# Performance work log

Hardware: AMD Instinct MI355X
Metric: run time of the kernel (lower is better)

Reference implementation:

```python
import jax, jax.numpy as jnp
import numpy as np
import math

K, T, B, N = 16, 40, 16, 32
BN = B * N


def _conv(x, w, b, stride):
    y = jax.lax.conv_general_dilated(x, w, (stride, stride), [(2, 2), (2, 2)],
                                     dimension_numbers=('NCHW', 'OIHW', 'NCHW'))
    return y + b[None, :, None, None]


def setup_inputs() -> dict:
    key = jax.random.key(0)
    ks = jax.random.split(key, 20)
    inp = {
        'hx': jax.random.normal(ks[0], (BN, 48), jnp.float32),
        'current_location': jax.random.uniform(ks[1], (BN, 2), jnp.float32, 0.0, 40.0),
        'y_path': jax.random.uniform(ks[2], (K, T, BN, 2), jnp.float32, 0.0, 40.0),
        'image_data': jax.random.normal(ks[3], (B, 4, 160, 160), jnp.float32),
        'conv1_w': jax.random.normal(ks[4], (16, 4, 5, 5), jnp.float32) * 0.1,
        'conv1_b': jax.random.normal(ks[5], (16,), jnp.float32) * 0.1,
        'conv2_w': jax.random.normal(ks[6], (32, 16, 5, 5), jnp.float32) * 0.05,
        'conv2_b': jax.random.normal(ks[7], (32,), jnp.float32) * 0.1,
        'fc_vel_w': jax.random.normal(ks[8], (16, 2), jnp.float32) * 0.1,
        'fc_vel_b': jax.random.normal(ks[9], (16,), jnp.float32) * 0.1,
        'fc_scf_w': jax.random.normal(ks[10], (48, 1728), jnp.float32) * 0.02,
        'fc_scf_b': jax.random.normal(ks[11], (48,), jnp.float32) * 0.1,
        'gru_w_ih': jax.random.normal(ks[12], (144, 96), jnp.float32) * 0.1,
        'gru_w_hh': jax.random.normal(ks[13], (144, 48), jnp.float32) * 0.1,
        'gru_b_ih': jax.random.normal(ks[14], (144,), jnp.float32) * 0.1,
        'gru_b_hh': jax.random.normal(ks[15], (144,), jnp.float32) * 0.1,
        'fc_dy_w': jax.random.normal(ks[16], (80, 48), jnp.float32) * 0.1,
        'fc_dy_b': jax.random.normal(ks[17], (80,), jnp.float32) * 0.1,
        'fc_score_w': jax.random.normal(ks[18], (1, 48), jnp.float32) * 0.1,
        'fc_score_b': jax.random.normal(ks[19], (1,), jnp.float32) * 0.1,
    }
    return inp


def reference(hx, current_location, y_path, image_data, conv1_w, conv1_b, conv2_w, conv2_b,
              fc_vel_w, fc_vel_b, fc_scf_w, fc_scf_b, gru_w_ih, gru_w_hh, gru_b_ih, gru_b_hh,
              fc_dy_w, fc_dy_b, fc_score_w, fc_score_b):
    k, t, bn, _ = y_path.shape
    b = image_data.shape[0]
    n = bn // b
    HZ = 10.0
    R0, R1 = 0.5, 4.0
    r_step = (R1 - R0) / 6.0
    th_step = 2.0 * math.pi / 6.0

    fmap = jax.nn.relu(_conv(jax.nn.relu(_conv(image_data, conv1_w, conv1_b, 2)), conv2_w, conv2_b, 1))  # (B,32,80,80)
    H, W = fmap.shape[2], fmap.shape[3]
    fm = fmap.transpose(0, 2, 3, 1)  # (B,H,W,32)

    # velocities (detached in original)
    vel = jnp.concatenate([y_path[:, :1] - current_location[None, None], jnp.diff(y_path, axis=1)], axis=1) * HZ
    vel = jax.lax.stop_gradient(vel)
    y_fv = vel @ fc_vel_w.T + fc_vel_b  # (K,T,bn,16)

    h0 = jnp.tile(hx, (k, 1))  # (K*bn,48)
    b_idx = jnp.arange(b)[None, :, None]
    eye = jnp.eye(n, dtype=bool)[None, None]

    def step(h, inp):
        path_t, fv_t = inp  # (K,bn,2), (K,bn,16)
        P = path_t.reshape(k, b, n, 2)  # bn index = batch*n + agent
        # map-feature gather at agent pixel
        u = jnp.clip(H // 2 - P[..., 1].astype(jnp.int32), 0, H - 1)
        v = jnp.clip(P[..., 0].astype(jnp.int32), 0, W - 1)
        feat = fm[b_idx, u, v]  # (K,B,N,32)
        # radius/theta binning (indices detached in original)
        Pd = jax.lax.stop_gradient(P)
        c = Pd[:, :, None, :, :] - Pd[:, :, :, None, :]  # c[k,b,j,t] = other_t - agent_j
        dist = jnp.linalg.norm(c, axis=-1)  # (K,B,N,N)
        mask = (dist >= R0) & (dist <= R1) & (~eye)
        dc = jnp.where(dist < 1e-10, 1e-10, dist)
        costh = jnp.arccos(jnp.clip(c[..., 0] / dc, -1.0, 1.0))
        theta = jnp.where(c[..., 1] < -0.01, 2.0 * math.pi - costh, costh)
        ub = jnp.clip(((dist - R0) / r_step).astype(jnp.int32), 0, 5)
        vb = jnp.clip((theta / th_step).astype(jnp.int32), 0, 5)
        bins = ub * 6 + vb  # (K,B,N,N) in [0,36)
        onehot = jax.nn.one_hot(bins, 36, dtype=h.dtype) * mask[..., None].astype(h.dtype)
        Hn = h[:bn].reshape(b, n, 48)  # original indexes only first bn rows of hidden
        sp = jnp.einsum('kbjto,bth->kbjoh', onehot, Hn)  # scatter-by-bin sum
        cnt = jnp.maximum(jnp.sum(onehot, axis=3), 1.0)
        sp = sp / jax.lax.stop_gradient(cnt)[..., None]
        sps = sp.reshape(k, bn, 36 * 48)
        lhalf = jnp.concatenate([feat, fv_t.reshape(k, b, n, 16)], axis=-1).reshape(k, bn, 48)
        rhalf = sps @ fc_scf_w.T + fc_scf_b
        x = jnp.concatenate([lhalf, rhalf], axis=-1).reshape(k * bn, 96)
        gi = x @ gru_w_ih.T + gru_b_ih
        gh = h @ gru_w_hh.T + gru_b_hh
        r = jax.nn.sigmoid(gi[:, :48] + gh[:, :48])
        z = jax.nn.sigmoid(gi[:, 48:96] + gh[:, 48:96])
        nn_ = jnp.tanh(gi[:, 96:] + r * gh[:, 96:])
        h_new = (1.0 - z) * nn_ + z * h
        return h_new, h_new

    path_seq = jnp.moveaxis(y_path, 1, 0)  # (T,K,bn,2)
    fv_seq = jnp.moveaxis(y_fv, 1, 0)
    h_final, hs = jax.lax.scan(step, h0, (path_seq, fv_seq))

    delta_y = (h_final @ fc_dy_w.T + fc_dy_b).reshape(k, bn, 2, t).transpose(0, 3, 1, 2)  # (K,T,bn,2)
    score = jnp.sum(hs @ fc_score_w.T + fc_score_b, axis=0).reshape(k, bn, 1)
    return delta_y, score
```

## Files before the change

### kernel.cpp

```cpp
#include <hip/hip_runtime.h>
#include <math.h>

typedef unsigned char u8;

#define KK 16
#define TT 40
#define BB 16
#define NN 32
#define BN 512
#define KBN 8192

#define OFF_FM   0u
#define OFF_C1   3276800u
#define OFF_W2T  4915200u
#define OFF_WT9  4928000u
#define OFF_WH3  4948736u
#define OFF_WGT  4951040u
#define OFF_H0   5033984u
#define OFF_H1   5427200u
#define OFF_SC   5820416u

__global__ __launch_bounds__(256) void k_init(const float* hx, float* h, float* score){
  int idx = blockIdx.x*256 + threadIdx.x;
  if (idx < KBN*48) h[idx] = hx[idx % (BN*48)];
  if (idx < KBN) score[idx] = 0.f;
}

__global__ __launch_bounds__(256) void k_prep(const float* conv2_w, const float* scfw,
                                              const float* wih, const float* whh,
                                              float* w2t, float* wt9g, float* wh3g, float* wgt_g){
  int idx = blockIdx.x*256 + threadIdx.x;
  if (idx < 12800) {
    int oc = idx & 31; int rest = idx >> 5;
    w2t[idx] = conv2_w[oc*400 + rest];
  }
  int i2 = idx - 12800;
  if (i2 >= 0 && i2 < 20736) {
    int kk2 = i2 / 144, rem = i2 % 144;
    int c = rem / 3, g = rem % 3;
    int o = g*48 + c;
    wt9g[i2] = (kk2 < 96) ? wih[o*96 + kk2] : whh[o*48 + (kk2 - 96)];
  }
  int i3 = idx - 33536;
  if (i3 >= 0 && i3 < 2304) {
    int kk2s = i3 / 48, c = i3 % 48;
    wh3g[i3] = whh[(96 + c)*48 + kk2s];
  }
  int i4 = idx - 35840;
  if (i4 >= 0 && i4 < 82944) {
    int bin = i4 / 2304, r2 = i4 % 2304;
    int hh = r2 / 48, cc = r2 % 48;
    wgt_g[i4] = scfw[cc*1728 + bin*48 + hh];
  }
}

__global__ __launch_bounds__(256) void k_conv1(const float* img, const float* w1, const float* b1, float* c1){
  int idx = blockIdx.x*256 + threadIdx.x;
  int ow = idx % 80, t1 = idx / 80;
  int oh = t1 % 80, t2 = t1 / 80;
  int oc = t2 % 16, b = t2 / 16;
  float acc = b1[oc];
  for (int ic = 0; ic < 4; ++ic)
    for (int kh = 0; kh < 5; ++kh) {
      int ih = oh*2 - 2 + kh;
      if (ih < 0 || ih >= 160) continue;
      const float* ip = img + ((b*4 + ic)*160 + ih)*160;
      const float* wp = w1 + ((oc*4 + ic)*5 + kh)*5;
      #pragma unroll
      for (int kw = 0; kw < 5; ++kw) {
        int iw = ow*2 - 2 + kw;
        if (iw >= 0 && iw < 160) acc += ip[iw] * wp[kw];
      }
    }
  c1[idx] = fmaxf(acc, 0.f);
}

__global__ __launch_bounds__(256) void k_conv2(const float* c1, const float* w2t, const float* b2, float* fm){
  int idx = blockIdx.x*256 + threadIdx.x;
  int oc = idx & 31;
  int t1 = idx >> 5;
  int owg = t1 % 20; int t2 = t1 / 20;
  int oh = t2 % 80; int b = t2 / 80;
  int ow0 = owg*4;
  float acc0=b2[oc],acc1=b2[oc],acc2=b2[oc],acc3=b2[oc];
  for (int ic = 0; ic < 16; ++ic)
    for (int kh = 0; kh < 5; ++kh) {
      int ih = oh - 2 + kh;
      if (ih < 0 || ih >= 80) continue;
      const float* ip = c1 + ((b*16 + ic)*80 + ih)*80;
      float cv[8];
      #pragma unroll
      for (int q = 0; q < 8; ++q) {
        int iw = ow0 - 2 + q;
        cv[q] = (iw >= 0 && iw < 80) ? ip[iw] : 0.f;
      }
      const float* wp = w2t + (ic*25 + kh*5)*32 + oc;
      #pragma unroll
      for (int kw = 0; kw < 5; ++kw) {
        float wv = wp[kw*32];
        acc0 += cv[kw]   * wv;
        acc1 += cv[kw+1] * wv;
        acc2 += cv[kw+2] * wv;
        acc3 += cv[kw+3] * wv;
      }
    }
  float* op = fm + ((b*80 + oh)*80 + ow0)*32 + oc;
  op[0]  = fmaxf(acc0, 0.f);
  op[32] = fmaxf(acc1, 0.f);
  op[64] = fmaxf(acc2, 0.f);
  op[96] = fmaxf(acc3, 0.f);
}

__global__ __launch_bounds__(256) void k_step2(
    const float* __restrict__ y_path, const float* __restrict__ cur_loc,
    const float* __restrict__ fm, const float* __restrict__ wgt,
    const float* __restrict__ wt9g,
    const float* __restrict__ vw, const float* __restrict__ vb2,
    const float* __restrict__ scfb, const float* __restrict__ bih,
    const float* __restrict__ bhh, const float* __restrict__ scw,
    const float* __restrict__ scb, const float* __restrict__ dyw,
    const float* __restrict__ dyb,
    const float* __restrict__ hin, float* __restrict__ hout,
    float* __restrict__ score, float* __restrict__ out, int t)
{
  __align__(16) __shared__ float wts[23040];
  __shared__ float X[32][148];
  __shared__ float HnL[32][49];
  __shared__ float PXs[32], PYs[32];
  __shared__ u8 BINM[32][32];
  __shared__ int PLE[1024];
  __shared__ float PWL[1024];
  __shared__ float SROW[32];
  __shared__ int lcnt;

  int tid = threadIdx.x;
  int row0 = blockIdx.x * 32;
  int kk = blockIdx.x >> 4;
  int bb = blockIdx.x & 15;

  {
    const float4* src = reinterpret_cast<const float4*>(wt9g);
    float4* dst = reinterpret_cast<float4*>(wts);
    for (int i = tid; i < 5760; i += 256) dst[i] = src[i];
  }
  for (int i = tid; i < 1536; i += 256) { int r = i/48, c = i%48; X[r][96+c] = hin[(row0+r)*48 + c]; }
  for (int i = tid; i < 1536; i += 256) { int r = i/48, c = i%48; HnL[r][c] = hin[(bb*32+r)*48 + c]; }
  if (tid < 32) {
    PXs[tid] = y_path[((kk*TT + t)*BN + bb*32 + tid)*2];
    PYs[tid] = y_path[((kk*TT + t)*BN + bb*32 + tid)*2 + 1];
    SROW[tid] = 0.f;
  }
  if (tid == 0) lcnt = 0;
  __syncthreads();

  for (int it2 = 0; it2 < 4; ++it2) {
    int p = tid + it2*256;
    int j = p >> 5, q = p & 31;
    float dx = PXs[q] - PXs[j], dy = PYs[q] - PYs[j];
    float dist = sqrtf(dx*dx + dy*dy);
    int bin = 255;
    if (q != j && dist >= 0.5f && dist <= 4.0f) {
      float ct = fminf(1.f, fmaxf(-1.f, dx / dist));
      float costh = acosf(ct);
      float theta = (dy < -0.01f) ? (6.28318530717958647692f - costh) : costh;
      int ub = (int)((dist - 0.5f) / 0.58333331346511840820f);
      ub = min(max(ub, 0), 5);
      int vb = (int)(theta / 1.04719758033752441406f);
      vb = min(max(vb, 0), 5);
      bin = ub*6 + vb;
    }
    BINM[j][q] = (u8)bin;
  }
  __syncthreads();

  for (int it2 = 0; it2 < 4; ++it2) {
    int p = tid + it2*256;
    int j = p >> 5, q = p & 31;
    int bq = BINM[j][q];
    if (bq != 255) {
      int cnt2 = 0;
      #pragma unroll
      for (int q2 = 0; q2 < 32; ++q2) cnt2 += (BINM[j][q2] == bq) ? 1 : 0;
      int idx2 = atomicAdd(&lcnt, 1);
      PLE[idx2] = (bq << 16) | (j << 8) | q;
      PWL[idx2] = 1.0f / (float)cnt2;
    }
  }
  for (int it2 = 0; it2 < 12; ++it2) {
    int task = tid + it2*256;
    int r = task / 96, c = task % 96;
    int rr = (row0 + r) & 511;
    float val;
    if (c < 32) {
      int u = min(max(40 - (int)PYs[r], 0), 79);
      int v = min(max((int)PXs[r], 0), 79);
      val = fm[((bb*80 + u)*80 + v)*32 + c];
    } else if (c < 48) {
      int o = c - 32;
      float qx, qy;
      if (t == 0) { qx = cur_loc[rr*2]; qy = cur_loc[rr*2 + 1]; }
      else { qx = y_path[((kk*TT + t - 1)*BN + rr)*2]; qy = y_path[((kk*TT + t - 1)*BN + rr)*2 + 1]; }
      float vx = (PXs[r] - qx)*10.f, vy = (PYs[r] - qy)*10.f;
      val = vx*vw[o*2] + vy*vw[o*2 + 1] + vb2[o];
    } else {
      val = scfb[c - 48];
    }
    X[r][c] = val;
  }
  __syncthreads();

  int P = lcnt;
  {
    int wid = tid >> 6, lane = tid & 63;
    if (lane < 48) {
      for (int p = wid; p < P; p += 4) {
        int e = PLE[p];
        int bin = e >> 16, j = (e >> 8) & 31, q = e & 31;
        float wv = PWL[p];
        const float* wp = wgt + bin*2304 + lane;
        float acc = 0.f;
        #pragma unroll
        for (int hh = 0; hh < 48; ++hh) acc += HnL[q][hh] * wp[hh*48];
        atomicAdd(&X[j][48 + lane], wv * acc);
      }
    }
  }
  __syncthreads();

  const float* wt9 = wts;
  const float* wh3 = wts + 20736;
  int tx = tid & 15, ty = tid >> 4;
  int r0 = ty*2;
  float a9[2][9], a3[2][3];
  #pragma unroll
  for (int ri = 0; ri < 2; ++ri) {
    #pragma unroll
    for (int m = 0; m < 9; ++m) a9[ri][m] = 0.f;
    #pragma unroll
    for (int m = 0; m < 3; ++m) a3[ri][m] = 0.f;
  }
  for (int k2 = 0; k2 < 144; ++k2) {
    float x0 = X[r0][k2], x1 = X[r0+1][k2];
    const float* wr = wt9 + k2*144 + 9*tx;
    #pragma unroll
    for (int m = 0; m < 9; ++m) {
      float wvm = wr[m];
      a9[0][m] += x0*wvm;
      a9[1][m] += x1*wvm;
    }
  }
  for (int k2 = 0; k2 < 48; ++k2) {
    float x0 = X[r0][96+k2], x1 = X[r0+1][96+k2];
    const float* wr = wh3 + k2*48 + 3*tx;
    #pragma unroll
    for (int m = 0; m < 3; ++m) {
      float wvm = wr[m];
      a3[0][m] += x0*wvm;
      a3[1][m] += x1*wvm;
    }
  }
  float hn[2][3];
  #pragma unroll
  for (int ri = 0; ri < 2; ++ri)
    #pragma unroll
    for (int c3 = 0; c3 < 3; ++c3) {
      int c = 3*tx + c3;
      float gR = a9[ri][3*c3+0] + bih[c]    + bhh[c];
      float gZ = a9[ri][3*c3+1] + bih[48+c] + bhh[48+c];
      float gN = a9[ri][3*c3+2] + bih[96+c] + bhh[96+c];
      float g3 = a3[ri][c3] + bhh[96+c];
      float rg = 1.f/(1.f + expf(-gR));
      float zg = 1.f/(1.f + expf(-gZ));
      float nn2 = tanhf(gN + (rg - 1.f)*g3);
      float hold = X[r0+ri][96+c];
      hn[ri][c3] = (1.f - zg)*nn2 + zg*hold;
    }
  __syncthreads();

  float sp0 = 0.f, sp1 = 0.f;
  #pragma unroll
  for (int c3 = 0; c3 < 3; ++c3) {
    int c = 3*tx + c3;
    X[r0][96+c]   = hn[0][c3];
    X[r0+1][96+c] = hn[1][c3];
    hout[(row0+r0)*48 + c]   = hn[0][c3];
    hout[(row0+r0+1)*48 + c] = hn[1][c3];
    sp0 += hn[0][c3]*scw[c];
    sp1 += hn[1][c3]*scw[c];
  }
  atomicAdd(&SROW[r0], sp0);
  atomicAdd(&SROW[r0+1], sp1);
  __syncthreads();

  if (tid < 32) {
    float s = score[row0 + tid] + SROW[tid] + scb[0];
    score[row0 + tid] = s;
    if (t == TT-1) out[KBN*80 + row0 + tid] = s;
  }
  if (t == TT-1) {
    for (int it2 = 0; it2 < 10; ++it2) {
      int task = tid + it2*256;
      int r = task / 80, c = task % 80;
      float acc = dyb[c];
      #pragma unroll
      for (int i = 0; i < 48; ++i) acc += X[r][96+i] * dyw[c*48 + i];
      int rr = (row0 + r) & 511;
      int d = c / 40, tq = c % 40;
      out[((kk*40 + tq)*512 + rr)*2 + d] = acc;
    }
  }
}

extern "C" void kernel_launch(void* const* d_in, const int* in_sizes, int n_in,
                              void* d_out, int out_size, void* d_ws, size_t ws_size,
                              hipStream_t stream)
{
  const float* hx   = (const float*)d_in[0];
  const float* cl   = (const float*)d_in[1];
  const float* yp   = (const float*)d_in[2];
  const float* img  = (const float*)d_in[3];
  const float* w1   = (const float*)d_in[4];
  const float* b1   = (const float*)d_in[5];
  const float* w2   = (const float*)d_in[6];
  const float* b2   = (const float*)d_in[7];
  const float* vw   = (const float*)d_in[8];
  const float* vb   = (const float*)d_in[9];
  const float* scfw = (const float*)d_in[10];
  const float* scfb = (const float*)d_in[11];
  const float* wih  = (const float*)d_in[12];
  const float* whh  = (const float*)d_in[13];
  const float* bih  = (const float*)d_in[14];
  const float* bhh  = (const float*)d_in[15];
  const float* dyw  = (const float*)d_in[16];
  const float* dyb  = (const float*)d_in[17];
  const float* scw  = (const float*)d_in[18];
  const float* scb  = (const float*)d_in[19];

  float* ws   = (float*)d_ws;
  float* fm   = ws + OFF_FM;
  float* c1   = ws + OFF_C1;
  float* w2t  = ws + OFF_W2T;
  float* wt9g = ws + OFF_WT9;
  float* wh3g = ws + OFF_WH3;
  float* wgtg = ws + OFF_WGT;
  float* hb0  = ws + OFF_H0;
  float* hb1  = ws + OFF_H1;
  float* sc   = ws + OFF_SC;
  float* out  = (float*)d_out;

  hipLaunchKernelGGL(k_init,  dim3(1536), dim3(256), 0, stream, hx, hb0, sc);
  hipLaunchKernelGGL(k_prep,  dim3(464),  dim3(256), 0, stream, w2, scfw, wih, whh, w2t, wt9g, wh3g, wgtg);
  hipLaunchKernelGGL(k_conv1, dim3(6400), dim3(256), 0, stream, img, w1, b1, c1);
  hipLaunchKernelGGL(k_conv2, dim3(3200), dim3(256), 0, stream, c1, w2t, b2, fm);
  for (int t = 0; t < TT; ++t) {
    float* hin  = (t & 1) ? hb1 : hb0;
    float* hout = (t & 1) ? hb0 : hb1;
    hipLaunchKernelGGL(k_step2, dim3(256), dim3(256), 0, stream,
        yp, cl, fm, wgtg, wt9g, vw, vb, scfb, bih, bhh, scw, scb, dyw, dyb, hin, hout, sc, out, t);
  }
}
```

Baseline: 1.761 ms.

## Fuse all GRU time steps into one persistent kernel with redundant k=0 chain

Replaces the 40 per-step launches with a single kernel that loops over time inside each block. Every step reads the hidden state of the k=0 rows, so each block now carries a second 32-row copy of that k=0 recurrence alongside its own rows. This removes the cross-block dependency, along with the global hidden-state ping-pong buffers and the init kernel. Weights and biases are loaded into shared memory once instead of every step, and the score is accumulated in registers. The cost is roughly twice the GRU and social-pooling arithmetic per block, plus higher register pressure from the 4-row tiles.

New measurement: 4.462 ms. +153.3%, slower.

```diff
diff --git a/kernel.cpp b/kernel.cpp
--- a/kernel.cpp
+++ b/kernel.cpp
@@ -16,15 +16,6 @@
 #define OFF_WT9  4928000u
 #define OFF_WH3  4948736u
 #define OFF_WGT  4951040u
-#define OFF_H0   5033984u
-#define OFF_H1   5427200u
-#define OFF_SC   5820416u
-
-__global__ __launch_bounds__(256) void k_init(const float* hx, float* h, float* score){
-  int idx = blockIdx.x*256 + threadIdx.x;
-  if (idx < KBN*48) h[idx] = hx[idx % (BN*48)];
-  if (idx < KBN) score[idx] = 0.f;
-}
 
 __global__ __launch_bounds__(256) void k_prep(const float* conv2_w, const float* scfw,
                                               const float* wih, const float* whh,
@@ -111,7 +102,7 @@
   op[96] = fmaxf(acc3, 0.f);
 }
 
-__global__ __launch_bounds__(256) void k_step2(
+__global__ __launch_bounds__(256) void k_seq(
     const float* __restrict__ y_path, const float* __restrict__ cur_loc,
     const float* __restrict__ fm, const float* __restrict__ wgt,
     const float* __restrict__ wt9g,
@@ -119,22 +110,20 @@
     const float* __restrict__ scfb, const float* __restrict__ bih,
     const float* __restrict__ bhh, const float* __restrict__ scw,
     const float* __restrict__ scb, const float* __restrict__ dyw,
-    const float* __restrict__ dyb,
-    const float* __restrict__ hin, float* __restrict__ hout,
-    float* __restrict__ score, float* __restrict__ out, int t)
+    const float* __restrict__ dyb, const float* __restrict__ hx,
+    float* __restrict__ out)
 {
   __align__(16) __shared__ float wts[23040];
-  __shared__ float X[32][148];
-  __shared__ float HnL[32][49];
-  __shared__ float PXs[32], PYs[32];
-  __shared__ u8 BINM[32][32];
-  __shared__ int PLE[1024];
-  __shared__ float PWL[1024];
+  __shared__ float X[64][148];
+  __shared__ float PX[2][32], PY[2][32];
+  __shared__ u8 BINM[2][32][32];
+  __shared__ int PLE[2048];
+  __shared__ float PWL[2048];
   __shared__ float SROW[32];
+  __shared__ float SV[432];
   __shared__ int lcnt;
 
   int tid = threadIdx.x;
-  int row0 = blockIdx.x * 32;
   int kk = blockIdx.x >> 4;
   int bb = blockIdx.x & 15;
 
@@ -143,171 +132,196 @@
     float4* dst = reinterpret_cast<float4*>(wts);
     for (int i = tid; i < 5760; i += 256) dst[i] = src[i];
   }
-  for (int i = tid; i < 1536; i += 256) { int r = i/48, c = i%48; X[r][96+c] = hin[(row0+r)*48 + c]; }
-  for (int i = tid; i < 1536; i += 256) { int r = i/48, c = i%48; HnL[r][c] = hin[(bb*32+r)*48 + c]; }
-  if (tid < 32) {
-    PXs[tid] = y_path[((kk*TT + t)*BN + bb*32 + tid)*2];
-    PYs[tid] = y_path[((kk*TT + t)*BN + bb*32 + tid)*2 + 1];
-    SROW[tid] = 0.f;
-  }
-  if (tid == 0) lcnt = 0;
+  for (int i = tid; i < 432; i += 256) {
+    float v;
+    if (i < 32) v = vw[i];
+    else if (i < 48) v = vb2[i-32];
+    else if (i < 96) v = scfb[i-48];
+    else if (i < 240) v = bih[i-96];
+    else if (i < 384) v = bhh[i-240];
+    else v = scw[i-384];
+    SV[i] = v;
+  }
+  for (int i = tid; i < 64*48; i += 256) {
+    int r = i/48, c = i%48;
+    X[r][96+c] = hx[(bb*32 + (r & 31))*48 + c];
+  }
+  if (tid < 32) SROW[tid] = 0.f;
+
+  int tx = tid & 15, ty = tid >> 4;
+  int r0 = ty*4;
+  float sacc[4] = {0.f, 0.f, 0.f, 0.f};
+
+  for (int t = 0; t < TT; ++t) {
+    __syncthreads();
+    if (tid < 64) {
+      int p = tid >> 5, j = tid & 31;
+      int kid = p ? kk : 0;
+      PX[p][j] = y_path[((kid*TT + t)*BN + bb*32 + j)*2];
+      PY[p][j] = y_path[((kid*TT + t)*BN + bb*32 + j)*2 + 1];
+    }
+    if (tid == 0) lcnt = 0;
+    __syncthreads();
+
+    for (int it2 = 0; it2 < 8; ++it2) {
+      int idx = tid + it2*256;
+      int p = idx >> 10, rem = idx & 1023;
+      int j = rem >> 5, q = rem & 31;
+      float dx = PX[p][q] - PX[p][j], dy = PY[p][q] - PY[p][j];
+      float dist = sqrtf(dx*dx + dy*dy);
+      int bin = 255;
+      if (q != j && dist >= 0.5f && dist <= 4.0f) {
+        float ct = fminf(1.f, fmaxf(-1.f, dx / dist));
+        float costh = acosf(ct);
+        float theta = (dy < -0.01f) ? (6.28318530717958647692f - costh) : costh;
+        int ub = (int)((dist - 0.5f) / 0.58333331346511840820f);
+        ub = min(max(ub, 0), 5);
+        int vb = (int)(theta / 1.04719758033752441406f);
+        vb = min(max(vb, 0), 5);
+        bin = ub*6 + vb;
+      }
+      BINM[p][j][q] = (u8)bin;
+    }
+    __syncthreads();
+
+    for (int it2 = 0; it2 < 8; ++it2) {
+      int idx = tid + it2*256;
+      int p = idx >> 10, rem = idx & 1023;
+      int j = rem >> 5, q = rem & 31;
+      int bq = BINM[p][j][q];
+      if (bq != 255) {
+        int cnt2 = 0;
+        #pragma unroll
+        for (int q2 = 0; q2 < 32; ++q2) cnt2 += (BINM[p][j][q2] == bq) ? 1 : 0;
+        int idx2 = atomicAdd(&lcnt, 1);
+        PLE[idx2] = (bq << 16) | ((p*32 + j) << 8) | q;
+        PWL[idx2] = 1.0f / (float)cnt2;
+      }
+    }
+    for (int it2 = 0; it2 < 24; ++it2) {
+      int task = tid + it2*256;
+      int r = task / 96, c = task % 96;
+      int p = r >> 5, j = r & 31;
+      float val;
+      if (c < 32) {
+        int u = min(max(40 - (int)PY[p][j], 0), 79);
+        int v = min(max((int)PX[p][j], 0), 79);
+        val = fm[((bb*80 + u)*80 + v)*32 + c];
+      } else if (c < 48) {
+        int o = c - 32;
+        int rr = bb*32 + j;
+        float qx, qy;
+        if (t == 0) { qx = cur_loc[rr*2]; qy = cur_loc[rr*2 + 1]; }
+        else {
+          int kid = p ? kk : 0;
+          qx = y_path[((kid*TT + t - 1)*BN + rr)*2];
+          qy = y_path[((kid*TT + t - 1)*BN + rr)*2 + 1];
+        }
+        float vx = (PX[p][j] - qx)*10.f, vy = (PY[p][j] - qy)*10.f;
+        val = vx*SV[o*2] + vy*SV[o*2 + 1] + SV[32 + o];
+      } else {
+        val = SV[c];
+      }
+      X[r][c] = val;
+    }
+    __syncthreads();
+
+    {
+      int P = lcnt;
+      int wid = tid >> 6, lane = tid & 63;
+      if (lane < 48) {
+        for (int p2 = wid; p2 < P; p2 += 4) {
+          int e = PLE[p2];
+          int bin = e >> 16, jf = (e >> 8) & 255, q = e & 255;
+          float wv = PWL[p2];
+          const float* wp = wgt + bin*2304 + lane;
+          float acc = 0.f;
+          #pragma unroll
+          for (int hh = 0; hh < 48; ++hh) acc += X[q][96+hh] * wp[hh*48];
+          atomicAdd(&X[jf][48 + lane], wv * acc);
+        }
+      }
+    }
+    __syncthreads();
+
+    float a9[4][9], a3[4][3];
+    #pragma unroll
+    for (int ri = 0; ri < 4; ++ri) {
+      #pragma unroll
+      for (int m = 0; m < 9; ++m) a9[ri][m] = 0.f;
+      #pragma unroll
+      for (int m = 0; m < 3; ++m) a3[ri][m] = 0.f;
+    }
+    for (int k2 = 0; k2 < 144; ++k2) {
+      float x0 = X[r0][k2], x1 = X[r0+1][k2], x2 = X[r0+2][k2], x3 = X[r0+3][k2];
+      const float* wr = wts + k2*144 + 9*tx;
+      #pragma unroll
+      for (int m = 0; m < 9; ++m) {
+        float wvm = wr[m];
+        a9[0][m] += x0*wvm;
+        a9[1][m] += x1*wvm;
+        a9[2][m] += x2*wvm;
+        a9[3][m] += x3*wvm;
+      }
+    }
+    for (int k2 = 0; k2 < 48; ++k2) {
+      float x0 = X[r0][96+k2], x1 = X[r0+1][96+k2], x2 = X[r0+2][96+k2], x3 = X[r0+3][96+k2];
+      const float* wr = wts + 20736 + k2*48 + 3*tx;
+      #pragma unroll
+      for (int m = 0; m < 3; ++m) {
+        float wvm = wr[m];
+        a3[0][m] += x0*wvm;
+        a3[1][m] += x1*wvm;
+        a3[2][m] += x2*wvm;
+        a3[3][m] += x3*wvm;
+      }
+    }
+    float hn[4][3];
+    #pragma unroll
+    for (int ri = 0; ri < 4; ++ri)
+      #pragma unroll
+      for (int c3 = 0; c3 < 3; ++c3) {
+        int c = 3*tx + c3;
+        float gR = a9[ri][3*c3+0] + SV[96+c]     + SV[240+c];
+        float gZ = a9[ri][3*c3+1] + SV[96+48+c]  + SV[240+48+c];
+        float gN = a9[ri][3*c3+2] + SV[96+96+c]  + SV[240+96+c];
+        float g3 = a3[ri][c3] + SV[240+96+c];
+        float rg = 1.f/(1.f + expf(-gR));
+        float zg = 1.f/(1.f + expf(-gZ));
+        float nn2 = tanhf(gN + (rg - 1.f)*g3);
+        float hold = X[r0+ri][96+c];
+        hn[ri][c3] = (1.f - zg)*nn2 + zg*hold;
+      }
+    __syncthreads();
+
+    #pragma unroll
+    for (int ri = 0; ri < 4; ++ri) {
+      float sp = 0.f;
+      #pragma unroll
+      for (int c3 = 0; c3 < 3; ++c3) {
+        int c = 3*tx + c3;
+        X[r0+ri][96+c] = hn[ri][c3];
+        sp += hn[ri][c3]*SV[384+c];
+      }
+      sacc[ri] += sp;
+    }
+  }
+  if (ty >= 8) {
+    #pragma unroll
+    for (int ri = 0; ri < 4; ++ri) atomicAdd(&SROW[r0 + ri - 32], sacc[ri]);
+  }
   __syncthreads();
 
-  for (int it2 = 0; it2 < 4; ++it2) {
-    int p = tid + it2*256;
-    int j = p >> 5, q = p & 31;
-    float dx = PXs[q] - PXs[j], dy = PYs[q] - PYs[j];
-    float dist = sqrtf(dx*dx + dy*dy);
-    int bin = 255;
-    if (q != j && dist >= 0.5f && dist <= 4.0f) {
-      float ct = fminf(1.f, fmaxf(-1.f, dx / dist));
-      float costh = acosf(ct);
-      float theta = (dy < -0.01f) ? (6.28318530717958647692f - costh) : costh;
-      int ub = (int)((dist - 0.5f) / 0.58333331346511840820f);
-      ub = min(max(ub, 0), 5);
-      int vb = (int)(theta / 1.04719758033752441406f);
-      vb = min(max(vb, 0), 5);
-      bin = ub*6 + vb;
-    }
-    BINM[j][q] = (u8)bin;
-  }
-  __syncthreads();
-
-  for (int it2 = 0; it2 < 4; ++it2) {
-    int p = tid + it2*256;
-    int j = p >> 5, q = p & 31;
-    int bq = BINM[j][q];
-    if (bq != 255) {
-      int cnt2 = 0;
-      #pragma unroll
-      for (int q2 = 0; q2 < 32; ++q2) cnt2 += (BINM[j][q2] == bq) ? 1 : 0;
-      int idx2 = atomicAdd(&lcnt, 1);
-      PLE[idx2] = (bq << 16) | (j << 8) | q;
-      PWL[idx2] = 1.0f / (float)cnt2;
-    }
-  }
-  for (int it2 = 0; it2 < 12; ++it2) {
+  if (tid < 32) out[KBN*80 + kk*512 + bb*32 + tid] = SROW[tid] + (float)TT * scb[0];
+  for (int it2 = 0; it2 < 10; ++it2) {
     int task = tid + it2*256;
-    int r = task / 96, c = task % 96;
-    int rr = (row0 + r) & 511;
-    float val;
-    if (c < 32) {
-      int u = min(max(40 - (int)PYs[r], 0), 79);
-      int v = min(max((int)PXs[r], 0), 79);
-      val = fm[((bb*80 + u)*80 + v)*32 + c];
-    } else if (c < 48) {
-      int o = c - 32;
-      float qx, qy;
-      if (t == 0) { qx = cur_loc[rr*2]; qy = cur_loc[rr*2 + 1]; }
-      else { qx = y_path[((kk*TT + t - 1)*BN + rr)*2]; qy = y_path[((kk*TT + t - 1)*BN + rr)*2 + 1]; }
-      float vx = (PXs[r] - qx)*10.f, vy = (PYs[r] - qy)*10.f;
-      val = vx*vw[o*2] + vy*vw[o*2 + 1] + vb2[o];
-    } else {
-      val = scfb[c - 48];
-    }
-    X[r][c] = val;
-  }
-  __syncthreads();
-
-  int P = lcnt;
-  {
-    int wid = tid >> 6, lane = tid & 63;
-    if (lane < 48) {
-      for (int p = wid; p < P; p += 4) {
-        int e = PLE[p];
-        int bin = e >> 16, j = (e >> 8) & 31, q = e & 31;
-        float wv = PWL[p];
-        const float* wp = wgt + bin*2304 + lane;
-        float acc = 0.f;
-        #pragma unroll
-        for (int hh = 0; hh < 48; ++hh) acc += HnL[q][hh] * wp[hh*48];
-        atomicAdd(&X[j][48 + lane], wv * acc);
-      }
-    }
-  }
-  __syncthreads();
-
-  const float* wt9 = wts;
-  const float* wh3 = wts + 20736;
-  int tx = tid & 15, ty = tid >> 4;
-  int r0 = ty*2;
-  float a9[2][9], a3[2][3];
-  #pragma unroll
-  for (int ri = 0; ri < 2; ++ri) {
-    #pragma unroll
-    for (int m = 0; m < 9; ++m) a9[ri][m] = 0.f;
-    #pragma unroll
-    for (int m = 0; m < 3; ++m) a3[ri][m] = 0.f;
-  }
-  for (int k2 = 0; k2 < 144; ++k2) {
-    float x0 = X[r0][k2], x1 = X[r0+1][k2];
-    const float* wr = wt9 + k2*144 + 9*tx;
-    #pragma unroll
-    for (int m = 0; m < 9; ++m) {
-      float wvm = wr[m];
-      a9[0][m] += x0*wvm;
-      a9[1][m] += x1*wvm;
-    }
-  }
-  for (int k2 = 0; k2 < 48; ++k2) {
-    float x0 = X[r0][96+k2], x1 = X[r0+1][96+k2];
-    const float* wr = wh3 + k2*48 + 3*tx;
-    #pragma unroll
-    for (int m = 0; m < 3; ++m) {
-      float wvm = wr[m];
-      a3[0][m] += x0*wvm;
-      a3[1][m] += x1*wvm;
-    }
-  }
-  float hn[2][3];
-  #pragma unroll
-  for (int ri = 0; ri < 2; ++ri)
-    #pragma unroll
-    for (int c3 = 0; c3 < 3; ++c3) {
-      int c = 3*tx + c3;
-      float gR = a9[ri][3*c3+0] + bih[c]    + bhh[c];
-      float gZ = a9[ri][3*c3+1] + bih[48+c] + bhh[48+c];
-      float gN = a9[ri][3*c3+2] + bih[96+c] + bhh[96+c];
-      float g3 = a3[ri][c3] + bhh[96+c];
-      float rg = 1.f/(1.f + expf(-gR));
-      float zg = 1.f/(1.f + expf(-gZ));
-      float nn2 = tanhf(gN + (rg - 1.f)*g3);
-      float hold = X[r0+ri][96+c];
-      hn[ri][c3] = (1.f - zg)*nn2 + zg*hold;
-    }
-  __syncthreads();
-
-  float sp0 = 0.f, sp1 = 0.f;
-  #pragma unroll
-  for (int c3 = 0; c3 < 3; ++c3) {
-    int c = 3*tx + c3;
-    X[r0][96+c]   = hn[0][c3];
-    X[r0+1][96+c] = hn[1][c3];
-    hout[(row0+r0)*48 + c]   = hn[0][c3];
-    hout[(row0+r0+1)*48 + c] = hn[1][c3];
-    sp0 += hn[0][c3]*scw[c];
-    sp1 += hn[1][c3]*scw[c];
-  }
-  atomicAdd(&SROW[r0], sp0);
-  atomicAdd(&SROW[r0+1], sp1);
-  __syncthreads();
-
-  if (tid < 32) {
-    float s = score[row0 + tid] + SROW[tid] + scb[0];
-    score[row0 + tid] = s;
-    if (t == TT-1) out[KBN*80 + row0 + tid] = s;
-  }
-  if (t == TT-1) {
-    for (int it2 = 0; it2 < 10; ++it2) {
-      int task = tid + it2*256;
-      int r = task / 80, c = task % 80;
-      float acc = dyb[c];
-      #pragma unroll
-      for (int i = 0; i < 48; ++i) acc += X[r][96+i] * dyw[c*48 + i];
-      int rr = (row0 + r) & 511;
-      int d = c / 40, tq = c % 40;
-      out[((kk*40 + tq)*512 + rr)*2 + d] = acc;
-    }
+    int r = task / 80, c = task % 80;
+    float acc = dyb[c];
+    #pragma unroll
+    for (int i = 0; i < 48; ++i) acc += X[32+r][96+i] * dyw[c*48 + i];
+    int rr = bb*32 + r;
+    int d = c / 40, tq = c % 40;
+    out[((kk*40 + tq)*512 + rr)*2 + d] = acc;
   }
 }
 
@@ -343,19 +357,12 @@
   float* wt9g = ws + OFF_WT9;
   float* wh3g = ws + OFF_WH3;
   float* wgtg = ws + OFF_WGT;
-  float* hb0  = ws + OFF_H0;
-  float* hb1  = ws + OFF_H1;
-  float* sc   = ws + OFF_SC;
   float* out  = (float*)d_out;
-
-  hipLaunchKernelGGL(k_init,  dim3(1536), dim3(256), 0, stream, hx, hb0, sc);
+  (void)wh3g;
+
   hipLaunchKernelGGL(k_prep,  dim3(464),  dim3(256), 0, stream, w2, scfw, wih, whh, w2t, wt9g, wh3g, wgtg);
   hipLaunchKernelGGL(k_conv1, dim3(6400), dim3(256), 0, stream, img, w1, b1, c1);
   hipLaunchKernelGGL(k_conv2, dim3(3200), dim3(256), 0, stream, c1, w2t, b2, fm);
-  for (int t = 0; t < TT; ++t) {
-    float* hin  = (t & 1) ? hb1 : hb0;
-    float* hout = (t & 1) ? hb0 : hb1;
-    hipLaunchKernelGGL(k_step2, dim3(256), dim3(256), 0, stream,
-        yp, cl, fm, wgtg, wt9g, vw, vb, scfb, bih, bhh, scw, scb, dyw, dyb, hin, hout, sc, out, t);
-  }
-}
+  hipLaunchKernelGGL(k_seq,   dim3(256),  dim3(256), 0, stream,
+      yp, cl, fm, wgtg, wt9g, vw, vb, scfb, bih, bhh, scw, scb, dyw, dyb, hx, out);
+}
```
